# Optimization experiments

Measured on AMD Instinct MI355X. Metric: run time of the kernel, lower is better.

## Reference

```python
import jax, jax.numpy as jnp
import numpy as np

THRESH = 0.3
PARTS = 6
D = 256
NHEAD = 8
DHEAD = 32
FF = 512
NLAYERS = 2
NUM_CLASSES = 396
EPS = 1e-5


def setup_inputs() -> dict:
    key = jax.random.key(0)
    ks = jax.random.split(key, 40)
    k = iter(ks)
    B, Q = 64, 300
    inp = {}
    inp["pred_logits"] = jax.random.normal(next(k), (B, Q, PARTS), jnp.float32)
    inp["hs"] = jax.random.normal(next(k), (B, Q, D), jnp.float32)
    for i, s in enumerate([96, 48, 24, 12]):
        inp[f"feat{i}"] = jax.random.normal(next(k), (B, D, s, s), jnp.float32)
    sc = 0.05
    inp["img_proj_w"] = sc * jax.random.normal(next(k), (4, D, D), jnp.float32)
    inp["img_proj_b"] = sc * jax.random.normal(next(k), (4, D), jnp.float32)
    inp["in_proj_w"] = sc * jax.random.normal(next(k), (NLAYERS, 3 * D, D), jnp.float32)
    inp["in_proj_b"] = sc * jax.random.normal(next(k), (NLAYERS, 3 * D), jnp.float32)
    inp["out_proj_w"] = sc * jax.random.normal(next(k), (NLAYERS, D, D), jnp.float32)
    inp["out_proj_b"] = sc * jax.random.normal(next(k), (NLAYERS, D), jnp.float32)
    inp["lin1_w"] = sc * jax.random.normal(next(k), (NLAYERS, FF, D), jnp.float32)
    inp["lin1_b"] = sc * jax.random.normal(next(k), (NLAYERS, FF), jnp.float32)
    inp["lin2_w"] = sc * jax.random.normal(next(k), (NLAYERS, D, FF), jnp.float32)
    inp["lin2_b"] = sc * jax.random.normal(next(k), (NLAYERS, D), jnp.float32)
    inp["ln1_w"] = jnp.ones((NLAYERS, D), jnp.float32)
    inp["ln1_b"] = jnp.zeros((NLAYERS, D), jnp.float32)
    inp["ln2_w"] = jnp.ones((NLAYERS, D), jnp.float32)
    inp["ln2_b"] = jnp.zeros((NLAYERS, D), jnp.float32)
    inp["cls1_w"] = sc * jax.random.normal(next(k), (512, D), jnp.float32)
    inp["cls1_b"] = sc * jax.random.normal(next(k), (512,), jnp.float32)
    inp["cls2_w"] = sc * jax.random.normal(next(k), (NUM_CLASSES, 512), jnp.float32)
    inp["cls2_b"] = sc * jax.random.normal(next(k), (NUM_CLASSES,), jnp.float32)
    return inp


def _layer_norm(x, w, b):
    m = jnp.mean(x, -1, keepdims=True)
    v = jnp.var(x, -1, keepdims=True)
    return (x - m) / jnp.sqrt(v + EPS) * w + b


def _forward(pred_logits, hs, feat0, feat1, feat2, feat3,
             img_proj_w, img_proj_b,
             in_proj_w, in_proj_b, out_proj_w, out_proj_b,
             lin1_w, lin1_b, lin2_w, lin2_b,
             ln1_w, ln1_b, ln2_w, ln2_b,
             cls1_w, cls1_b, cls2_w, cls2_b):
    B = hs.shape[0]
    # --- per-class masked mean pooling over queries (vectorized segment-mean) ---
    pred = jax.nn.sigmoid(pred_logits)                       # [B,Q,P]
    cmask = (pred > THRESH).astype(hs.dtype)                 # [B,Q,P]
    counts = cmask.sum(1)                                    # [B,P]
    csum = jnp.einsum("bqp,bqd->bpd", cmask, hs)             # [B,P,D]
    cmean = csum / jnp.maximum(counts, 1.0)[..., None]
    valid_c = counts > 0                                     # [B,P] bool
    any_valid = valid_c.any(1)                               # [B]
    # fallback: batches with no active class use hs[b, :1] in slot 0
    slot0 = jnp.where(any_valid[:, None], cmean[:, 0], hs[:, 0])
    cmean = cmean.at[:, 0].set(slot0)
    valid_c = valid_c.at[:, 0].set(valid_c[:, 0] | ~any_valid)
    # --- image tokens: global average pool + per-scale linear proj ---
    img_toks = jnp.stack([
        feat.mean((2, 3)) @ img_proj_w[i].T + img_proj_b[i]
        for i, feat in enumerate([feat0, feat1, feat2, feat3])
    ], axis=1)                                               # [B,4,D]
    tokens = jnp.concatenate([cmean, img_toks], 1)           # [B,L,D], L=PARTS+4
    valid = jnp.concatenate(
        [valid_c, jnp.ones((B, 4), bool)], 1)                # [B,L]
    NEG = jnp.asarray(-1e30, tokens.dtype)
    bias = jnp.where(valid, 0.0, NEG)[:, None, None, :]      # [B,1,1,L] key padding
    L = tokens.shape[1]
    x = tokens
    # --- 2-layer post-norm transformer encoder (eval mode, no dropout) ---
    for l in range(NLAYERS):
        qkv = x @ in_proj_w[l].T + in_proj_b[l]
        q, k_, v = jnp.split(qkv, 3, -1)
        q = q.reshape(B, L, NHEAD, DHEAD)
        k_ = k_.reshape(B, L, NHEAD, DHEAD)
        v = v.reshape(B, L, NHEAD, DHEAD)
        scores = jnp.einsum("bqhd,bkhd->bhqk", q, k_) / np.sqrt(DHEAD).astype(np.float32)
        attn = jax.nn.softmax(scores + bias, -1)
        ao = jnp.einsum("bhqk,bkhd->bqhd", attn, v).reshape(B, L, D)
        ao = ao @ out_proj_w[l].T + out_proj_b[l]
        x = _layer_norm(x + ao, ln1_w[l], ln1_b[l])
        ff = jax.nn.relu(x @ lin1_w[l].T + lin1_b[l]) @ lin2_w[l].T + lin2_b[l]
        x = _layer_norm(x + ff, ln2_w[l], ln2_b[l])
    # --- masked mean pool over valid tokens + classifier ---
    vf = valid.astype(x.dtype)
    lengths = jnp.maximum(vf.sum(1, keepdims=True), 1.0)
    cls_tok = (x * vf[..., None]).sum(1) / lengths           # [B,D]
    h = jax.nn.relu(cls_tok @ cls1_w.T + cls1_b)
    logits = h @ cls2_w.T + cls2_b                           # [B,NUM_CLASSES]
    return logits


def reference(pred_logits, hs, feat0, feat1, feat2, feat3,
              img_proj_w, img_proj_b,
              in_proj_w, in_proj_b, out_proj_w, out_proj_b,
              lin1_w, lin1_b, lin2_w, lin2_b,
              ln1_w, ln1_b, ln2_w, ln2_b,
              cls1_w, cls1_b, cls2_w, cls2_b):
    return _forward(pred_logits, hs, feat0, feat1, feat2, feat3,
                    img_proj_w, img_proj_b,
                    in_proj_w, in_proj_b, out_proj_w, out_proj_b,
                    lin1_w, lin1_b, lin2_w, lin2_b,
                    ln1_w, ln1_b, ln2_w, ln2_b,
                    cls1_w, cls1_b, cls2_w, cls2_b)
```

## Files before the change

### kernel.cpp

```cpp
#include <hip/hip_runtime.h>
#include <hip/hip_fp16.h>
#include <math.h>

#define NB 64
#define NQ 300
#define NP 6
#define ND 256
#define NF 512
#define NCL 396
#define NT 10

#define IPW_OFF 0
#define INW_OFF 262144
#define OW_OFF  655360
#define L1W_OFF 786432
#define L2W_OFF 1048576
#define C1W_OFF 1310720
#define C2W_OFF 1441792
#define TOTW    1644544
#define CONV_BLOCKS 803
#define POOL_ROWS 65536

typedef float f4 __attribute__((ext_vector_type(4)));

__device__ __forceinline__ float wred(float s) {
    #pragma unroll
    for (int o = 32; o; o >>= 1) s += __shfl_down(s, o, 64);
    return s;
}

__device__ __forceinline__ float dot8h(f4 wv, f4 xlo, f4 xhi) {
    const __half2* hp = reinterpret_cast<const __half2*>(&wv);
    float2 p0 = __half22float2(hp[0]);
    float2 p1 = __half22float2(hp[1]);
    float2 p2 = __half22float2(hp[2]);
    float2 p3 = __half22float2(hp[3]);
    return p0.x * xlo.x + p0.y * xlo.y + p1.x * xlo.z + p1.y * xlo.w
         + p2.x * xhi.x + p2.y * xhi.y + p3.x * xhi.z + p3.y * xhi.w;
}

__device__ __forceinline__ void qsync(int* flag, int tid) {
    __syncthreads();
    if (tid == 0) {
        __threadfence();
        __hip_atomic_fetch_add(flag, 1, __ATOMIC_ACQ_REL, __HIP_MEMORY_SCOPE_AGENT);
        while (__hip_atomic_load(flag, __ATOMIC_ACQUIRE, __HIP_MEMORY_SCOPE_AGENT) < 4)
            __builtin_amdgcn_s_sleep(2);
    }
    __syncthreads();
}

__global__ __launch_bounds__(256) void pool_cls_kernel(
    const float* __restrict__ pred, const float* __restrict__ hs,
    const float* __restrict__ f0, const float* __restrict__ f1,
    const float* __restrict__ f2, const float* __restrict__ f3,
    const float* __restrict__ ipw, const float* __restrict__ inw,
    const float* __restrict__ ow, const float* __restrict__ l1w,
    const float* __restrict__ l2w, const float* __restrict__ c1w,
    const float* __restrict__ c2w,
    float* __restrict__ pooled, float* __restrict__ tokG,
    float* __restrict__ biasW, __half* __restrict__ wH,
    int* __restrict__ flagW)
{
    const int bid = blockIdx.x;
    const int tid = threadIdx.x;
    __shared__ float shm[1824];

    if (bid < NB) {
        const int b = bid;
        if (tid < 16) flagW[b * 16 + tid] = 0;
        float* maskL = shm;
        float* countsL = shm + 1800;
        for (int i = tid; i < NQ * NP; i += 256) {
            float x = pred[(size_t)b * NQ * NP + i];
            float sg = 1.f / (1.f + expf(-x));
            maskL[i] = (sg > 0.3f) ? 1.f : 0.f;
        }
        __syncthreads();
        if (tid < NP) {
            float c = 0.f;
            for (int q = 0; q < NQ; q++) c += maskL[q * NP + tid];
            countsL[tid] = c;
        }
        __syncthreads();
        float acc[NP] = {0.f, 0.f, 0.f, 0.f, 0.f, 0.f};
        const float* hsb = hs + (size_t)b * NQ * ND + tid;
        for (int q = 0; q < NQ; q++) {
            float h = hsb[(size_t)q * ND];
            #pragma unroll
            for (int p = 0; p < NP; p++) acc[p] += maskL[q * NP + p] * h;
        }
        bool anyv = false;
        #pragma unroll
        for (int p = 0; p < NP; p++) anyv = anyv || (countsL[p] > 0.f);
        #pragma unroll
        for (int p = 0; p < NP; p++) {
            float cm = acc[p] / fmaxf(countsL[p], 1.f);
            if (p == 0 && !anyv) cm = hs[(size_t)b * NQ * ND + tid];
            tokG[(size_t)b * 2560 + p * ND + tid] = cm;
        }
        if (tid < 16) {
            float bv = 0.f;
            if (tid < NP) {
                bool v = countsL[tid] > 0.f;
                if (tid == 0 && !anyv) v = true;
                bv = v ? 0.f : -1e30f;
            }
            biasW[b * 16 + tid] = bv;
        }
        return;
    }

    if (bid >= NB + POOL_ROWS) {
        const int cid = bid - (NB + POOL_ROWS);
        size_t base = (size_t)cid * 2048 + (size_t)tid * 8;
        const float* src; size_t off;
        if      (base < INW_OFF) { src = ipw; off = IPW_OFF; }
        else if (base < OW_OFF)  { src = inw; off = INW_OFF; }
        else if (base < L1W_OFF) { src = ow;  off = OW_OFF;  }
        else if (base < L2W_OFF) { src = l1w; off = L1W_OFF; }
        else if (base < C1W_OFF) { src = l2w; off = L2W_OFF; }
        else if (base < C2W_OFF) { src = c1w; off = C1W_OFF; }
        else                     { src = c2w; off = C2W_OFF; }
        const f4* s4 = reinterpret_cast<const f4*>(src + (base - off));
        f4 a = s4[0], b2 = s4[1];
        union { __half2 h[4]; f4 v; } u;
        u.h[0] = __floats2half2_rn(a.x, a.y);
        u.h[1] = __floats2half2_rn(a.z, a.w);
        u.h[2] = __floats2half2_rn(b2.x, b2.y);
        u.h[3] = __floats2half2_rn(b2.z, b2.w);
        *reinterpret_cast<f4*>(wH + base) = u.v;
        return;
    }

    const int row = bid - NB;
    const int scale = row >> 14;
    const int rr = row & 16383;
    const int b = rr >> 8;
    const int d = rr & 255;
    const float* src;
    int n;
    switch (scale) {
        case 0: src = f0; n = 96 * 96; break;
        case 1: src = f1; n = 48 * 48; break;
        case 2: src = f2; n = 24 * 24; break;
        default: src = f3; n = 12 * 12; break;
    }
    const f4* p4 = reinterpret_cast<const f4*>(src + ((size_t)b * ND + d) * (size_t)n);
    int n4 = n >> 2;
    float s = 0.f;
    for (int i = tid; i < n4; i += 256) {
        f4 v = __builtin_nontemporal_load(&p4[i]);
        s += v.x + v.y + v.z + v.w;
    }
    s = wred(s);
    int wid = tid >> 6, lane = tid & 63;
    if (lane == 0) shm[wid] = s;
    __syncthreads();
    if (tid == 0) {
        float t = shm[0] + shm[1] + shm[2] + shm[3];
        pooled[((size_t)b * 4 + scale) * ND + d] = t / (float)n;
    }
}

__global__ __launch_bounds__(512) void xform_kernel(
    const float* __restrict__ pooled, float* tokG,
    const float* __restrict__ biasW, const __half* __restrict__ wH,
    const float* __restrict__ ipb, const float* __restrict__ inb,
    const float* __restrict__ ob, const float* __restrict__ l1b,
    const float* __restrict__ l2b,
    const float* __restrict__ n1w, const float* __restrict__ n1b,
    const float* __restrict__ n2w, const float* __restrict__ n2b,
    const float* __restrict__ c1b, const float* __restrict__ c2b,
    float* opW, float* f2W, float* hW,
    int* flagW, float* __restrict__ out)
{
    const int b  = blockIdx.x & 63;
    const int qt = blockIdx.x >> 6;
    const int tid = threadIdx.x;
    const int lane = tid & 63;
    const int wv = tid >> 6;
    int* flags = flagW + b * 16;

    __shared__ __align__(16) float xs[2560];
    __shared__ __align__(16) float loc[1920];
    __shared__ __align__(16) float res[2560];
    __shared__ __align__(16) float h1a[1280];
    __shared__ __align__(16) float pp[3840];
    __shared__ float sc[224];
    __shared__ float stats[32];
    __shared__ float biasK[16];

    const f4* xs4 = reinterpret_cast<const f4*>(xs);
    const f4* loc4 = reinterpret_cast<const f4*>(loc);
    const f4* res4 = reinterpret_cast<const f4*>(res);
    const f4* h1a4 = reinterpret_cast<const f4*>(h1a);

    for (int i = tid; i < 1024; i += 512) loc[i] = pooled[(size_t)b * 1024 + i];
    if (tid < 16) biasK[tid] = biasW[b * 16 + tid];
    __syncthreads();

    if (tid < 256) {
        const int i = tid >> 6, cl = tid & 63;
        const int c = qt * 64 + cl;
        const f4* w4 = reinterpret_cast<const f4*>(wH + IPW_OFF + ((size_t)(i * 256 + c)) * 256);
        float acc = 0.f;
        #pragma unroll 4
        for (int k8 = 0; k8 < 32; k8++)
            acc += dot8h(w4[k8], loc4[i * 64 + 2 * k8], loc4[i * 64 + 2 * k8 + 1]);
        tokG[(size_t)b * 2560 + (6 + i) * 256 + c] = acc + ipb[i * 256 + c];
    }
    qsync(&flags[0], tid);
    for (int i = tid; i < 2560; i += 512) xs[i] = tokG[(size_t)b * 2560 + i];
    __syncthreads();

    for (int l = 0; l < 2; l++) {
        if (tid < 384) {
            const int ks = tid / 192, cl = tid % 192;
            const int m = cl >> 6;
            const int gc = m * 256 + qt * 64 + (cl & 63);
            const f4* w4 = reinterpret_cast<const f4*>(wH + INW_OFF + ((size_t)l * 768 + gc) * 256 + ks * 128);
            float acc[NT];
            #pragma unroll
            for (int r = 0; r < NT; r++) acc[r] = 0.f;
            for (int k8 = 0; k8 < 16; k8++) {
                f4 wv4 = w4[k8];
                const int xi = ks * 32 + 2 * k8;
                #pragma unroll
                for (int r = 0; r < NT; r++)
                    acc[r] += dot8h(wv4, xs4[r * 64 + xi], xs4[r * 64 + xi + 1]);
            }
            #pragma unroll
            for (int r = 0; r < NT; r++) pp[ks * 1920 + r * 192 + cl] = acc[r];
        }
        __syncthreads();
        for (int i = tid; i < 1920; i += 512) {
            int r = i / 192, cl = i - r * 192;
            int m = cl >> 6, gc = m * 256 + qt * 64 + (cl & 63);
            loc[i] = pp[i] + pp[1920 + i] + inb[l * 768 + gc];
        }
        __syncthreads();

        if (tid < 200) {
            int hl = tid / 100, rem = tid - 100 * hl;
            int qr = rem / 10, kr = rem - 10 * qr;
            const float* qp = &loc[qr * 192 + hl * 32];
            const float* kp = &loc[kr * 192 + 64 + hl * 32];
            float s = 0.f;
            #pragma unroll
            for (int d = 0; d < 32; d++) s += qp[d] * kp[d];
            sc[tid] = s * 0.17677669529663687f + biasK[kr];
        }
        __syncthreads();
        if (tid < 20) {
            float* row = &sc[tid * 10];
            float m = row[0];
            #pragma unroll
            for (int k = 1; k < 10; k++) m = fmaxf(m, row[k]);
            float ss = 0.f;
            #pragma unroll
            for (int k = 0; k < 10; k++) { float e = expf(row[k] - m); row[k] = e; ss += e; }
            float inv = 1.f / ss;
            #pragma unroll
            for (int k = 0; k < 10; k++) row[k] *= inv;
        }
        __syncthreads();

        for (int idx = tid; idx < 640; idx += 512) {
            int hl = idx / 320, rem = idx - 320 * hl;
            int r = rem >> 5, c = rem & 31;
            float s = 0.f;
            #pragma unroll
            for (int kr = 0; kr < 10; kr++)
                s += sc[hl * 100 + r * 10 + kr] * loc[kr * 192 + 128 + hl * 32 + c];
            h1a[r * 64 + hl * 32 + c] = s;
        }
        __syncthreads();

        {
            const int c = tid & 255, rh = tid >> 8;
            const f4* w4 = reinterpret_cast<const f4*>(wH + OW_OFF + ((size_t)l * 256 + c) * 256 + qt * 64);
            float acc[5];
            #pragma unroll
            for (int rr = 0; rr < 5; rr++) acc[rr] = 0.f;
            for (int k8 = 0; k8 < 8; k8++) {
                f4 wv4 = w4[k8];
                #pragma unroll
                for (int rr = 0; rr < 5; rr++) {
                    int r = rh * 5 + rr;
                    acc[rr] += dot8h(wv4, h1a4[r * 16 + 2 * k8], h1a4[r * 16 + 2 * k8 + 1]);
                }
            }
            #pragma unroll
            for (int rr = 0; rr < 5; rr++)
                opW[((size_t)(b * 4 + qt)) * 2560 + (rh * 5 + rr) * 256 + c] = acc[rr];
        }
        qsync(&flags[1 + 2 * l], tid);

        for (int i = tid; i < 2560; i += 512) {
            float v = opW[(size_t)(b * 4 + 0) * 2560 + i] + opW[(size_t)(b * 4 + 1) * 2560 + i]
                    + opW[(size_t)(b * 4 + 2) * 2560 + i] + opW[(size_t)(b * 4 + 3) * 2560 + i]
                    + ob[l * 256 + (i & 255)] + xs[i];
            res[i] = v;
        }
        __syncthreads();
        for (int r = wv; r < NT; r += 8) {
            float v0 = res[r * 256 + lane], v1 = res[r * 256 + 64 + lane];
            float v2 = res[r * 256 + 128 + lane], v3 = res[r * 256 + 192 + lane];
            float s = wred(v0 + v1 + v2 + v3);
            float q = wred(v0 * v0 + v1 * v1 + v2 * v2 + v3 * v3);
            if (lane == 0) {
                float m = s * (1.f / 256.f);
                stats[r] = m;
                stats[16 + r] = rsqrtf(fmaxf(q * (1.f / 256.f) - m * m, 0.f) + 1e-5f);
            }
        }
        __syncthreads();
        for (int i = tid; i < 2560; i += 512) {
            int r = i >> 8, c = i & 255;
            xs[i] = (res[i] - stats[r]) * stats[16 + r] * n1w[l * 256 + c] + n1b[l * 256 + c];
        }
        __syncthreads();

        if (tid < 256) {
            const int cl = tid & 127, rh = (tid >> 7) & 1;
            const int gc = qt * 128 + cl;
            const f4* w4 = reinterpret_cast<const f4*>(wH + L1W_OFF + ((size_t)l * 512 + gc) * 256);
            float acc[5];
            #pragma unroll
            for (int rr = 0; rr < 5; rr++) acc[rr] = 0.f;
            for (int k8 = 0; k8 < 32; k8++) {
                f4 wv4 = w4[k8];
                #pragma unroll
                for (int rr = 0; rr < 5; rr++) {
                    int r = rh * 5 + rr;
                    acc[rr] += dot8h(wv4, xs4[r * 64 + 2 * k8], xs4[r * 64 + 2 * k8 + 1]);
                }
            }
            float bb = l1b[l * 512 + gc];
            #pragma unroll
            for (int rr = 0; rr < 5; rr++)
                h1a[(rh * 5 + rr) * 128 + cl] = fmaxf(acc[rr] + bb, 0.f);
        }
        __syncthreads();

        {
            const int c = tid & 255, rh = tid >> 8;
            const f4* w4 = reinterpret_cast<const f4*>(wH + L2W_OFF + ((size_t)l * 256 + c) * 512 + qt * 128);
            float acc[5];
            #pragma unroll
            for (int rr = 0; rr < 5; rr++) acc[rr] = 0.f;
            for (int k8 = 0; k8 < 16; k8++) {
                f4 wv4 = w4[k8];
                #pragma unroll
                for (int rr = 0; rr < 5; rr++) {
                    int r = rh * 5 + rr;
                    acc[rr] += dot8h(wv4, h1a4[r * 32 + 2 * k8], h1a4[r * 32 + 2 * k8 + 1]);
                }
            }
            #pragma unroll
            for (int rr = 0; rr < 5; rr++)
                f2W[((size_t)(b * 4 + qt)) * 2560 + (rh * 5 + rr) * 256 + c] = acc[rr];
        }
        qsync(&flags[2 + 2 * l], tid);

        for (int i = tid; i < 2560; i += 512) {
            float v = f2W[(size_t)(b * 4 + 0) * 2560 + i] + f2W[(size_t)(b * 4 + 1) * 2560 + i]
                    + f2W[(size_t)(b * 4 + 2) * 2560 + i] + f2W[(size_t)(b * 4 + 3) * 2560 + i]
                    + l2b[l * 256 + (i & 255)] + xs[i];
            res[i] = v;
        }
        __syncthreads();
        for (int r = wv; r < NT; r += 8) {
            float v0 = res[r * 256 + lane], v1 = res[r * 256 + 64 + lane];
            float v2 = res[r * 256 + 128 + lane], v3 = res[r * 256 + 192 + lane];
            float s = wred(v0 + v1 + v2 + v3);
            float q = wred(v0 * v0 + v1 * v1 + v2 * v2 + v3 * v3);
            if (lane == 0) {
                float m = s * (1.f / 256.f);
                stats[r] = m;
                stats[16 + r] = rsqrtf(fmaxf(q * (1.f / 256.f) - m * m, 0.f) + 1e-5f);
            }
        }
        __syncthreads();
        for (int i = tid; i < 2560; i += 512) {
            int r = i >> 8, c = i & 255;
            xs[i] = (res[i] - stats[r]) * stats[16 + r] * n2w[l * 256 + c] + n2b[l * 256 + c];
        }
        __syncthreads();
    }

    if (tid < 256) {
        float len = 0.f, s = 0.f;
        #pragma unroll
        for (int r = 0; r < NT; r++) {
            float v = (biasK[r] == 0.f) ? 1.f : 0.f;
            len += v;
            s += v * xs[r * 256 + tid];
        }
        res[tid] = s / fmaxf(len, 1.f);
    }
    __syncthreads();

    if (tid < 256) {
        const int kh = tid >> 7, cl = tid & 127;
        const int gc = qt * 128 + cl;
        const f4* w4 = reinterpret_cast<const f4*>(wH + C1W_OFF + (size_t)gc * 256 + kh * 128);
        float acc = 0.f;
        #pragma unroll 4
        for (int k8 = 0; k8 < 16; k8++)
            acc += dot8h(w4[k8], res4[kh * 32 + 2 * k8], res4[kh * 32 + 2 * k8 + 1]);
        pp[kh * 128 + cl] = acc;
    }
    __syncthreads();
    if (tid < 128) {
        const int gc = qt * 128 + tid;
        hW[(size_t)b * 512 + gc] = fmaxf(pp[tid] + pp[128 + tid] + c1b[gc], 0.f);
    }
    qsync(&flags[5], tid);
    for (int i = tid; i < 512; i += 512) res[i] = hW[(size_t)b * 512 + i];
    __syncthreads();

    if (tid < 99) {
        const int o = qt * 99 + tid;
        const f4* w4 = reinterpret_cast<const f4*>(wH + C2W_OFF + (size_t)o * 512);
        float acc = 0.f;
        #pragma unroll 4
        for (int k8 = 0; k8 < 64; k8++)
            acc += dot8h(w4[k8], res4[2 * k8], res4[2 * k8 + 1]);
        out[(size_t)b * NCL + o] = acc + c2b[o];
    }
}

extern "C" void kernel_launch(void* const* d_in, const int* in_sizes, int n_in,
                              void* d_out, int out_size, void* d_ws, size_t ws_size,
                              hipStream_t stream)
{
    const float* pred = (const float*)d_in[0];
    const float* hs   = (const float*)d_in[1];
    const float* f0   = (const float*)d_in[2];
    const float* f1   = (const float*)d_in[3];
    const float* f2   = (const float*)d_in[4];
    const float* f3   = (const float*)d_in[5];
    const float* ipw  = (const float*)d_in[6];
    const float* ipb  = (const float*)d_in[7];
    const float* inw  = (const float*)d_in[8];
    const float* inb  = (const float*)d_in[9];
    const float* ow   = (const float*)d_in[10];
    const float* ob   = (const float*)d_in[11];
    const float* l1w  = (const float*)d_in[12];
    const float* l1b  = (const float*)d_in[13];
    const float* l2w  = (const float*)d_in[14];
    const float* l2b  = (const float*)d_in[15];
    const float* ln1w = (const float*)d_in[16];
    const float* ln1b = (const float*)d_in[17];
    const float* ln2w = (const float*)d_in[18];
    const float* ln2b = (const float*)d_in[19];
    const float* c1w  = (const float*)d_in[20];
    const float* c1b  = (const float*)d_in[21];
    const float* c2w  = (const float*)d_in[22];
    const float* c2b  = (const float*)d_in[23];

    float* ws = (float*)d_ws;
    float* pooled = ws;
    float* tokG   = pooled + NB * 4 * ND;
    float* biasW  = tokG + NB * 2560;
    __half* wH    = (__half*)(biasW + 1024);
    float* opW    = (float*)(wH + TOTW);
    float* f2W    = opW + NB * 4 * 2560;
    float* hW     = f2W + NB * 4 * 2560;
    int*   flagW  = (int*)(hW + NB * 512);

    pool_cls_kernel<<<NB + POOL_ROWS + CONV_BLOCKS, 256, 0, stream>>>(
        pred, hs, f0, f1, f2, f3, ipw, inw, ow, l1w, l2w, c1w, c2w,
        pooled, tokG, biasW, wH, flagW);
    xform_kernel<<<4 * NB, 512, 0, stream>>>(
        pooled, tokG, biasW, wH, ipb, inb, ob, l1b, l2b,
        ln1w, ln1b, ln2w, ln2b, c1b, c2b,
        opW, f2W, hW, flagW, (float*)d_out);
}
```

Baseline: 283.0 us.

## Compute image projection and classifier hidden layer redundantly per block to drop grid syncs

Each of the four blocks per batch now computes all four image-projection tokens and the full 512-wide first classifier layer locally in shared memory, instead of splitting the columns across blocks and exchanging them through global memory. This removes two of the inter-block flag syncs and their global round trips. In exchange each block does four times the work in those two stages, and the flag indices are renumbered to match.

```diff
diff --git a/kernel.cpp b/kernel.cpp
--- a/kernel.cpp
+++ b/kernel.cpp
@@ -97,7 +97,7 @@
         for (int p = 0; p < NP; p++) {
             float cm = acc[p] / fmaxf(countsL[p], 1.f);
             if (p == 0 && !anyv) cm = hs[(size_t)b * NQ * ND + tid];
-            tokG[(size_t)b * 2560 + p * ND + tid] = cm;
+            tokG[(size_t)b * 1536 + p * ND + tid] = cm;
         }
         if (tid < 16) {
             float bv = 0.f;
@@ -164,7 +164,7 @@
 }
 
 __global__ __launch_bounds__(512) void xform_kernel(
-    const float* __restrict__ pooled, float* tokG,
+    const float* __restrict__ pooled, const float* __restrict__ tokG,
     const float* __restrict__ biasW, const __half* __restrict__ wH,
     const float* __restrict__ ipb, const float* __restrict__ inb,
     const float* __restrict__ ob, const float* __restrict__ l1b,
@@ -172,7 +172,7 @@
     const float* __restrict__ n1w, const float* __restrict__ n1b,
     const float* __restrict__ n2w, const float* __restrict__ n2b,
     const float* __restrict__ c1b, const float* __restrict__ c2b,
-    float* opW, float* f2W, float* hW,
+    float* opW, float* f2W,
     int* flagW, float* __restrict__ out)
 {
     const int b  = blockIdx.x & 63;
@@ -196,22 +196,20 @@
     const f4* res4 = reinterpret_cast<const f4*>(res);
     const f4* h1a4 = reinterpret_cast<const f4*>(h1a);
 
+    for (int i = tid; i < 1536; i += 512) xs[i] = tokG[(size_t)b * 1536 + i];
     for (int i = tid; i < 1024; i += 512) loc[i] = pooled[(size_t)b * 1024 + i];
     if (tid < 16) biasK[tid] = biasW[b * 16 + tid];
     __syncthreads();
 
-    if (tid < 256) {
-        const int i = tid >> 6, cl = tid & 63;
-        const int c = qt * 64 + cl;
+    for (int idx = tid; idx < 1024; idx += 512) {
+        const int i = idx >> 8, c = idx & 255;
         const f4* w4 = reinterpret_cast<const f4*>(wH + IPW_OFF + ((size_t)(i * 256 + c)) * 256);
         float acc = 0.f;
         #pragma unroll 4
         for (int k8 = 0; k8 < 32; k8++)
             acc += dot8h(w4[k8], loc4[i * 64 + 2 * k8], loc4[i * 64 + 2 * k8 + 1]);
-        tokG[(size_t)b * 2560 + (6 + i) * 256 + c] = acc + ipb[i * 256 + c];
-    }
-    qsync(&flags[0], tid);
-    for (int i = tid; i < 2560; i += 512) xs[i] = tokG[(size_t)b * 2560 + i];
+        xs[(6 + i) * 256 + c] = acc + ipb[i * 256 + c];
+    }
     __syncthreads();
 
     for (int l = 0; l < 2; l++) {
@@ -295,7 +293,7 @@
             for (int rr = 0; rr < 5; rr++)
                 opW[((size_t)(b * 4 + qt)) * 2560 + (rh * 5 + rr) * 256 + c] = acc[rr];
         }
-        qsync(&flags[1 + 2 * l], tid);
+        qsync(&flags[0 + 2 * l], tid);
 
         for (int i = tid; i < 2560; i += 512) {
             float v = opW[(size_t)(b * 4 + 0) * 2560 + i] + opW[(size_t)(b * 4 + 1) * 2560 + i]
@@ -362,7 +360,7 @@
             for (int rr = 0; rr < 5; rr++)
                 f2W[((size_t)(b * 4 + qt)) * 2560 + (rh * 5 + rr) * 256 + c] = acc[rr];
         }
-        qsync(&flags[2 + 2 * l], tid);
+        qsync(&flags[1 + 2 * l], tid);
 
         for (int i = tid; i < 2560; i += 512) {
             float v = f2W[(size_t)(b * 4 + 0) * 2560 + i] + f2W[(size_t)(b * 4 + 1) * 2560 + i]
@@ -402,32 +400,27 @@
     }
     __syncthreads();
 
-    if (tid < 256) {
-        const int kh = tid >> 7, cl = tid & 127;
-        const int gc = qt * 128 + cl;
-        const f4* w4 = reinterpret_cast<const f4*>(wH + C1W_OFF + (size_t)gc * 256 + kh * 128);
+    {
+        const int c = tid;
+        const f4* w4 = reinterpret_cast<const f4*>(wH + C1W_OFF + (size_t)c * 256);
         float acc = 0.f;
         #pragma unroll 4
-        for (int k8 = 0; k8 < 16; k8++)
-            acc += dot8h(w4[k8], res4[kh * 32 + 2 * k8], res4[kh * 32 + 2 * k8 + 1]);
-        pp[kh * 128 + cl] = acc;
-    }
-    __syncthreads();
-    if (tid < 128) {
-        const int gc = qt * 128 + tid;
-        hW[(size_t)b * 512 + gc] = fmaxf(pp[tid] + pp[128 + tid] + c1b[gc], 0.f);
-    }
-    qsync(&flags[5], tid);
-    for (int i = tid; i < 512; i += 512) res[i] = hW[(size_t)b * 512 + i];
+        for (int k8 = 0; k8 < 32; k8++)
+            acc += dot8h(w4[k8], res4[2 * k8], res4[2 * k8 + 1]);
+        float hv = fmaxf(acc + c1b[c], 0.f);
+        __syncthreads();
+        res[512 + c] = hv;
+    }
     __syncthreads();
 
     if (tid < 99) {
         const int o = qt * 99 + tid;
         const f4* w4 = reinterpret_cast<const f4*>(wH + C2W_OFF + (size_t)o * 512);
+        const f4* h4 = reinterpret_cast<const f4*>(res + 512);
         float acc = 0.f;
         #pragma unroll 4
         for (int k8 = 0; k8 < 64; k8++)
-            acc += dot8h(w4[k8], res4[2 * k8], res4[2 * k8 + 1]);
+            acc += dot8h(w4[k8], h4[2 * k8], h4[2 * k8 + 1]);
         out[(size_t)b * NCL + o] = acc + c2b[o];
     }
 }
@@ -464,12 +457,11 @@
     float* ws = (float*)d_ws;
     float* pooled = ws;
     float* tokG   = pooled + NB * 4 * ND;
-    float* biasW  = tokG + NB * 2560;
+    float* biasW  = tokG + NB * 1536;
     __half* wH    = (__half*)(biasW + 1024);
     float* opW    = (float*)(wH + TOTW);
     float* f2W    = opW + NB * 4 * 2560;
-    float* hW     = f2W + NB * 4 * 2560;
-    int*   flagW  = (int*)(hW + NB * 512);
+    int*   flagW  = (int*)(f2W + NB * 4 * 2560);
 
     pool_cls_kernel<<<NB + POOL_ROWS + CONV_BLOCKS, 256, 0, stream>>>(
         pred, hs, f0, f1, f2, f3, ipw, inw, ow, l1w, l2w, c1w, c2w,
@@ -477,5 +469,5 @@
     xform_kernel<<<4 * NB, 512, 0, stream>>>(
         pooled, tokG, biasW, wH, ipb, inb, ob, l1b, l2b,
         ln1w, ln1b, ln2w, ln2b, c1b, c2b,
-        opW, f2W, hW, flagW, (float*)d_out);
-}
+        opW, f2W, flagW, (float*)d_out);
+}
```

After: 278.3 us. About the same (-1.7%).
